# Kernel tuning notes

Measured on AMD Instinct MI355X. Metric: run time of the kernel, lower is better.

## Reference

```python
import jax, jax.numpy as jnp
import numpy as np
from jax import lax

# Static problem configuration (SAModule(ratio=0.25, r=0.2, MLP([35,64,64,128])))
B, N, C_IN = 8, 4096, 32
RATIO, R, K = 0.25, 0.2, 64   # K == max_num_neighbors
M = int(N * RATIO)            # centroids per cloud after FPS
NEG = -1e10


def setup_inputs() -> dict:
    key = jax.random.key(0)
    ks = jax.random.split(key, 6)
    x = jax.random.normal(ks[0], (B * N, C_IN), jnp.float32)
    pos = jax.random.uniform(ks[1], (B * N, 3), jnp.float32)  # unit cube -> r=0.2 balls are non-trivial
    batch = jnp.repeat(jnp.arange(B, dtype=jnp.int32), N)
    def lin(k, fan_in, fan_out):
        return jax.random.normal(k, (fan_in, fan_out), jnp.float32) * (1.0 / np.sqrt(fan_in))
    W1 = lin(ks[2], C_IN + 3, 64); b1 = jnp.zeros((64,), jnp.float32)
    W2 = lin(ks[3], 64, 64);       b2 = jnp.zeros((64,), jnp.float32)
    W3 = lin(ks[4], 64, 128);      b3 = jnp.zeros((128,), jnp.float32)
    return {"x": x, "pos": pos, "batch": batch,
            "W1": W1, "b1": b1, "W2": W2, "b2": b2, "W3": W3, "b3": b3}


def _fps_one(p):
    """Farthest-point sampling on one cloud p:[N,3] -> idx:[M] (deterministic start at 0)."""
    def body(carry, _):
        dmin, last = carry
        d = jnp.sum((p - p[last]) ** 2, axis=-1)         # [N] sq-dist to last picked point
        dmin = jnp.minimum(dmin, d)
        nxt = jnp.argmax(dmin).astype(jnp.int32)
        return (dmin, nxt), nxt
    init = (jnp.full((N,), 1e10, jnp.float32), jnp.int32(0))
    _, rest = lax.scan(body, init, None, length=M - 1)
    return jnp.concatenate([jnp.zeros((1,), jnp.int32), rest])


def _sa_one(p, xb, ib, W1, b1, W2, b2, W3, b3):
    """Radius ball-query + PointNetConv (gather -> MLP -> masked scatter-max) on one cloud."""
    ctr = p[ib]                                              # [M,3] sampled centroids
    d2 = jnp.sum((ctr[:, None, :] - p[None, :, :]) ** 2, -1)  # [M,N]
    negd, nbr = lax.top_k(-d2, K)                            # K nearest per centroid
    valid = (-negd) <= R * R                                 # inside-ball mask [M,K]
    xj = xb[nbr]                                             # [M,K,C_IN] gathered features
    rel = p[nbr] - ctr[:, None, :]                           # [M,K,3] relative positions
    h = jnp.concatenate([xj, rel], axis=-1)                  # message input [x_j, pos_j - pos_i]
    h = jax.nn.relu(h @ W1 + b1)
    h = jax.nn.relu(h @ W2 + b2)
    h = h @ W3 + b3                                          # plain last layer (PyG MLP plain_last)
    h = jnp.where(valid[..., None], h, NEG)
    return jnp.max(h, axis=1)                                # max aggregation -> [M,128]


def reference(x, pos, batch, W1, b1, W2, b2, W3, b3):
    pos3 = pos.reshape(B, N, 3)
    x3 = x.reshape(B, N, C_IN)
    idx = jax.vmap(_fps_one)(pos3)                           # [B,M]
    conv = lambda p, xb, ib: _sa_one(p, xb, ib, W1, b1, W2, b2, W3, b3)
    x_out = jax.vmap(conv)(pos3, x3, idx)                    # [B,M,128]
    pos_out = jnp.take_along_axis(pos3, idx[..., None], axis=1)  # [B,M,3]
    batch_out = jnp.repeat(jnp.arange(B, dtype=batch.dtype), M)
    return x_out.reshape(B * M, -1), pos_out.reshape(B * M, 3), batch_out
```

## Files before the change

kernel.cpp:

```cpp
#include <hip/hip_runtime.h>
#include <hip/hip_bf16.h>

#define BB 8
#define NN 4096
#define CIN 32
#define MM 1024
#define KNB 64
#define CAND 1024
#define ROWS 72
#define GRID 256
#define NWORK (GRID - 8)

typedef __attribute__((ext_vector_type(8))) short  short8;
typedef __attribute__((ext_vector_type(4))) float  f32x4;
typedef __attribute__((ext_vector_type(2))) float  f32x2;

__device__ __forceinline__ float sq3(float dx, float dy, float dz) {
    return __fadd_rn(__fadd_rn(__fmul_rn(dx, dx), __fmul_rn(dy, dy)), __fmul_rn(dz, dz));
}

__device__ __forceinline__ unsigned short f2bf(float v) {
    union { __hip_bfloat16 b; unsigned short u; } cv;
    cv.b = __float2bfloat16(v);
    return cv.u;
}
__device__ __forceinline__ float bf2f(unsigned short u) {
    union { unsigned short u; __hip_bfloat16 b; } cv;
    cv.u = u;
    return __bfloat162float(cv.b);
}

static __device__ __forceinline__ f32x4 mfma16(short8 a, short8 b, f32x4 c) {
    return __builtin_amdgcn_mfma_f32_16x16x32_bf16(a, b, c, 0, 0, 0);
}

template<int CTRL>
__device__ __forceinline__ unsigned long long dpp_maxkey(unsigned long long k) {
    unsigned int lo = (unsigned int)k;
    unsigned int hi = (unsigned int)(k >> 32);
    unsigned int nlo = (unsigned int)__builtin_amdgcn_update_dpp((int)lo, (int)lo, CTRL, 0xF, 0xF, false);
    unsigned int nhi = (unsigned int)__builtin_amdgcn_update_dpp((int)hi, (int)hi, CTRL, 0xF, 0xF, false);
    unsigned long long nk = ((unsigned long long)nhi << 32) | (unsigned long long)nlo;
    return nk > k ? nk : k;
}

__global__ __launch_bounds__(256) void prep_kernel(
    const float* __restrict__ W1, const float* __restrict__ W2,
    const float* __restrict__ W3, unsigned short* __restrict__ wf)
{
    int gid = blockIdx.x * 256 + threadIdx.x;
    const float* W; int K, Ncol, base, slot;
    if (gid < 1024)      { W = W1; K = 35; Ncol = 64;  base = 0;     slot = gid; }
    else if (gid < 2048) { W = W2; K = 64; Ncol = 64;  base = 8192;  slot = gid - 1024; }
    else                 { W = W3; K = 64; Ncol = 128; base = 16384; slot = gid - 2048; }
    int lane = slot & 63, h = (slot >> 6) & 1, kstep = (slot >> 7) & 1, tile = slot >> 8;
    int col = tile * 16 + (lane & 15), quad = lane >> 4;
#pragma unroll
    for (int j = 0; j < 8; ++j) {
        int k = kstep * 32 + quad * 8 + j;
        float wv = (k < K) ? W[k * Ncol + col] : 0.0f;
        unsigned short hi = f2bf(wv);
        unsigned short v = h ? f2bf(wv - bf2f(hi)) : hi;
        wf[base + slot * 8 + j] = v;
    }
}

struct SaShared {
    unsigned short HA[2 * 64 * ROWS];
    unsigned long long candk[CAND];
    int   cnt;
    int   ok;
    int   sel[KNB];
    float red[4][128];
};

__device__ __forceinline__ void sa_process(
    SaShared& sh, const float* __restrict__ x, const float* __restrict__ P,
    const unsigned short* __restrict__ wf,
    const float* __restrict__ b1, const float* __restrict__ b2,
    const float* __restrict__ b3, float* __restrict__ out, int bm, int b, int ci)
{
    const int t    = threadIdx.x;
    const int w    = t >> 6;
    const int lane = t & 63;
    const float R2 = (float)(0.2 * 0.2);

    if (t == 0) sh.cnt = 0;
    __syncthreads();

    const float cx = P[3 * ci], cy = P[3 * ci + 1], cz = P[3 * ci + 2];

    for (int i = t; i < NN; i += 256) {
        float dx = P[3 * i] - cx, dy = P[3 * i + 1] - cy, dz = P[3 * i + 2] - cz;
        float d2 = sq3(dx, dy, dz);
        bool hit = d2 <= R2;
        unsigned long long mk = __ballot(hit);
        if (mk) {
            int leader = __ffsll((unsigned long long)mk) - 1;
            int base = 0;
            if (lane == leader) base = atomicAdd(&sh.cnt, __popcll(mk));
            base = __shfl(base, leader);
            if (hit) {
                int p = base + __popcll(mk & ((1ull << lane) - 1));
                if (p < CAND)
                    sh.candk[p] = ((unsigned long long)__float_as_uint(d2) << 32)
                                | (unsigned int)i;
            }
        }
    }
    __syncthreads();
    const int n = min(sh.cnt, CAND);
    const int V = min(n, KNB);

    for (int i = t; i < n; i += 256) {
        unsigned long long ki = sh.candk[i];
        int rank = 0;
        for (int j = 0; j < n; ++j)
            rank += (sh.candk[j] < ki) ? 1 : 0;
        if (rank < KNB) sh.sel[rank] = (int)(ki & 0xffffffffu);
    }
    __syncthreads();

    {
        const int row = 16 * w + (lane & 15);
        const int prt = lane >> 4;
        short8 z = {};
        *(short8*)(sh.HA + row * ROWS + 32 + prt * 8) = z;
        *(short8*)(sh.HA + 64 * ROWS + row * ROWS + 32 + prt * 8) = z;
        if (row < V) {
            int g = b * NN + sh.sel[row];
            const float4* xr = (const float4*)(x + (size_t)g * CIN + prt * 8);
            float4 v0 = xr[0], v1 = xr[1];
            float vv[8] = {v0.x, v0.y, v0.z, v0.w, v1.x, v1.y, v1.z, v1.w};
            short8 hv, lv;
#pragma unroll
            for (int j = 0; j < 8; ++j) {
                unsigned short h = f2bf(vv[j]);
                hv[j] = (short)h;
                lv[j] = (short)f2bf(vv[j] - bf2f(h));
            }
            *(short8*)(sh.HA + row * ROWS + prt * 8) = hv;
            *(short8*)(sh.HA + 64 * ROWS + row * ROWS + prt * 8) = lv;
            if (prt == 0) {
                int g2 = sh.sel[row];
#pragma unroll
                for (int c = 0; c < 3; ++c) {
                    float cc = (c == 0) ? cx : (c == 1) ? cy : cz;
                    float rv = P[3 * g2 + c] - cc;
                    unsigned short h = f2bf(rv);
                    sh.HA[row * ROWS + 32 + c] = h;
                    sh.HA[64 * ROWS + row * ROWS + 32 + c] = f2bf(rv - bf2f(h));
                }
            }
        }
    }

    const int m16  = lane & 15;
    const int quad = lane >> 4;
    const int arow = 16 * w + m16;
    const short8* wf8 = (const short8*)wf;

    {
        short8 aH[2], aL[2];
        aH[0] = *(const short8*)(sh.HA + arow * ROWS + quad * 8);
        aH[1] = *(const short8*)(sh.HA + arow * ROWS + 32 + quad * 8);
        aL[0] = *(const short8*)(sh.HA + 64 * ROWS + arow * ROWS + quad * 8);
        aL[1] = *(const short8*)(sh.HA + 64 * ROWS + arow * ROWS + 32 + quad * 8);
#pragma unroll
        for (int tile = 0; tile < 4; ++tile) {
            f32x4 acc = {};
#pragma unroll
            for (int ks = 0; ks < 2; ++ks) {
                short8 bH = wf8[((tile * 2 + ks) * 2 + 0) * 64 + lane];
                short8 bL = wf8[((tile * 2 + ks) * 2 + 1) * 64 + lane];
                acc = mfma16(aH[ks], bH, acc);
                acc = mfma16(aH[ks], bL, acc);
                acc = mfma16(aL[ks], bH, acc);
            }
            int col = tile * 16 + m16;
            float bb = b1[col];
#pragma unroll
            for (int i = 0; i < 4; ++i) {
                int grow = 16 * w + quad * 4 + i;
                float v = fmaxf(acc[i] + bb, 0.0f);
                unsigned short h = f2bf(v);
                sh.HA[grow * ROWS + col] = h;
                sh.HA[64 * ROWS + grow * ROWS + col] = f2bf(v - bf2f(h));
            }
        }
    }

    {
        short8 aH[2], aL[2];
        aH[0] = *(const short8*)(sh.HA + arow * ROWS + quad * 8);
        aH[1] = *(const short8*)(sh.HA + arow * ROWS + 32 + quad * 8);
        aL[0] = *(const short8*)(sh.HA + 64 * ROWS + arow * ROWS + quad * 8);
        aL[1] = *(const short8*)(sh.HA + 64 * ROWS + arow * ROWS + 32 + quad * 8);
#pragma unroll
        for (int tile = 0; tile < 4; ++tile) {
            f32x4 acc = {};
#pragma unroll
            for (int ks = 0; ks < 2; ++ks) {
                short8 bH = wf8[1024 + ((tile * 2 + ks) * 2 + 0) * 64 + lane];
                short8 bL = wf8[1024 + ((tile * 2 + ks) * 2 + 1) * 64 + lane];
                acc = mfma16(aH[ks], bH, acc);
                acc = mfma16(aH[ks], bL, acc);
                acc = mfma16(aL[ks], bH, acc);
            }
            int col = tile * 16 + m16;
            float bb = b2[col];
#pragma unroll
            for (int i = 0; i < 4; ++i) {
                int grow = 16 * w + quad * 4 + i;
                float v = fmaxf(acc[i] + bb, 0.0f);
                unsigned short h = f2bf(v);
                sh.HA[grow * ROWS + col] = h;
                sh.HA[64 * ROWS + grow * ROWS + col] = f2bf(v - bf2f(h));
            }
        }
    }

    {
        short8 aH[2], aL[2];
        aH[0] = *(const short8*)(sh.HA + arow * ROWS + quad * 8);
        aH[1] = *(const short8*)(sh.HA + arow * ROWS + 32 + quad * 8);
        aL[0] = *(const short8*)(sh.HA + 64 * ROWS + arow * ROWS + quad * 8);
        aL[1] = *(const short8*)(sh.HA + 64 * ROWS + arow * ROWS + 32 + quad * 8);
#pragma unroll
        for (int tile = 0; tile < 8; ++tile) {
            f32x4 acc = {};
#pragma unroll
            for (int ks = 0; ks < 2; ++ks) {
                short8 bH = wf8[2048 + ((tile * 2 + ks) * 2 + 0) * 64 + lane];
                short8 bL = wf8[2048 + ((tile * 2 + ks) * 2 + 1) * 64 + lane];
                acc = mfma16(aH[ks], bH, acc);
                acc = mfma16(aH[ks], bL, acc);
                acc = mfma16(aL[ks], bH, acc);
            }
            float mv = -1e10f;
#pragma unroll
            for (int i = 0; i < 4; ++i) {
                int grow = 16 * w + quad * 4 + i;
                float v = (grow < V) ? acc[i] : -1e10f;
                mv = fmaxf(mv, v);
            }
            mv = fmaxf(mv, __shfl_xor(mv, 16));
            mv = fmaxf(mv, __shfl_xor(mv, 32));
            if (lane < 16) sh.red[w][tile * 16 + lane] = mv;
        }
    }
    __syncthreads();

    if (t < 128) {
        float v = fmaxf(fmaxf(sh.red[0][t], sh.red[1][t]),
                        fmaxf(sh.red[2][t], sh.red[3][t]));
        out[(size_t)bm * 128 + t] = v + b3[t];
    }
}

union SharedMem {
    struct {
        float4 plds4[NN];
        int    chosen[MM];
        __align__(16) unsigned long long part[2][4];
    } fps;
    SaShared sa;
    char occupancy_pad[86016];
};

__global__ __launch_bounds__(256, 1) void fused_kernel(
    const float* __restrict__ x, const float* __restrict__ pos,
    int* __restrict__ idx_ws, unsigned int* __restrict__ ready,
    int* __restrict__ done, const unsigned short* __restrict__ wf,
    const float* __restrict__ b1, const float* __restrict__ b2,
    const float* __restrict__ b3, float* __restrict__ out)
{
    __shared__ SharedMem sh;
    const int t = threadIdx.x;

    if (blockIdx.x < BB) {
        __builtin_amdgcn_s_setprio(3);
        const int b = blockIdx.x;
        const float* P = pos + (size_t)b * NN * 3;
        for (int i = t; i < NN; i += 256) {
            float4 v;
            v.x = P[3 * i]; v.y = P[3 * i + 1]; v.z = P[3 * i + 2]; v.w = 0.0f;
            sh.fps.plds4[i] = v;
        }
        if (t == 0) {
            sh.fps.chosen[0] = 0;
            __hip_atomic_store(&idx_ws[b * MM], 0, __ATOMIC_RELAXED,
                               __HIP_MEMORY_SCOPE_AGENT);
        }
        __syncthreads();

        f32x2 pxv[8], pyv[8], pzv[8], dminv[8];
#pragma unroll
        for (int s = 0; s < 8; ++s) {
            float4 a = sh.fps.plds4[t + 512 * s];
            float4 c = sh.fps.plds4[t + 512 * s + 256];
            pxv[s] = (f32x2){a.x, c.x};
            pyv[s] = (f32x2){a.y, c.y};
            pzv[s] = (f32x2){a.z, c.z};
            dminv[s] = (f32x2){1e10f, 1e10f};
        }

        int win = 0;
        for (int it = 1; it < MM; ++it) {
            float4 wc = sh.fps.plds4[win];
            const f32x2 lxv = (f32x2){wc.x, wc.x};
            const f32x2 lyv = (f32x2){wc.y, wc.y};
            const f32x2 lzv = (f32x2){wc.z, wc.z};
            float bv = -1.0f;
            int   bi = 0;
#pragma unroll
            for (int s = 0; s < 8; ++s) {
                f32x2 d;
                {
#pragma clang fp contract(off)
                    f32x2 dx = pxv[s] - lxv;
                    f32x2 dy = pyv[s] - lyv;
                    f32x2 dz = pzv[s] - lzv;
                    d = dx * dx + dy * dy + dz * dz;
                }
                float m0 = fminf(dminv[s].x, d.x);
                float m1 = fminf(dminv[s].y, d.y);
                dminv[s].x = m0;
                dminv[s].y = m1;
                if (m0 > bv) { bv = m0; bi = t + 512 * s; }
                if (m1 > bv) { bv = m1; bi = t + 512 * s + 256; }
            }
            unsigned long long k =
                ((unsigned long long)__float_as_uint(bv) << 32) | (unsigned int)(~bi);
            k = dpp_maxkey<0x111>(k);
            k = dpp_maxkey<0x112>(k);
            k = dpp_maxkey<0x114>(k);
            k = dpp_maxkey<0x118>(k);
            k = dpp_maxkey<0x142>(k);
            k = dpp_maxkey<0x143>(k);
            if ((t & 63) == 63) sh.fps.part[it & 1][t >> 6] = k;
            __syncthreads();
            const ulonglong2* pp = (const ulonglong2*)&sh.fps.part[it & 1][0];
            ulonglong2 p01 = pp[0], p23 = pp[1];
            unsigned long long ka = p01.x > p01.y ? p01.x : p01.y;
            unsigned long long kb = p23.x > p23.y ? p23.x : p23.y;
            unsigned long long km = ka > kb ? ka : kb;
            win = (int)(~(unsigned int)km);
            if (t == 0) {
                sh.fps.chosen[it] = win;
                __hip_atomic_store(&idx_ws[b * MM + it], win, __ATOMIC_RELAXED,
                                   __HIP_MEMORY_SCOPE_AGENT);
                if ((it & 31) == 31)
                    __hip_atomic_store(&ready[b], (unsigned int)(it + 1),
                                       __ATOMIC_RELEASE, __HIP_MEMORY_SCOPE_AGENT);
            }
        }
        __syncthreads();

        for (int m = t; m < MM; m += 256) {
            int mi = sh.fps.chosen[m];
            const int PO = BB * MM * 128;
            const int BO = PO + BB * MM * 3;
            int row = b * MM + m;
            float4 c = sh.fps.plds4[mi];
            out[PO + 3 * row + 0] = c.x;
            out[PO + 3 * row + 1] = c.y;
            out[PO + 3 * row + 2] = c.z;
            out[BO + row] = (float)b;
        }
        return;
    }

    int budget = 8000;
    for (int item = (int)blockIdx.x - BB; item < BB * MM; item += NWORK) {
        const int m  = item >> 3;
        const int b  = item & 7;
        const int bm = b * MM + m;
        const float* P = pos + (size_t)b * NN * 3;

        if (t == 0) {
            const unsigned int need = (unsigned int)(m + 1);
            while (budget > 0 &&
                   __hip_atomic_load(&ready[b], __ATOMIC_ACQUIRE,
                                     __HIP_MEMORY_SCOPE_AGENT) < need) {
                __builtin_amdgcn_s_sleep(10);
                --budget;
            }
            sh.sa.ok = (__hip_atomic_load(&ready[b], __ATOMIC_ACQUIRE,
                                          __HIP_MEMORY_SCOPE_AGENT) >= need) ? 1 : 0;
        }
        __syncthreads();
        const int myok = sh.sa.ok;
        __syncthreads();
        if (!myok) continue;

        const int ci = __hip_atomic_load(&idx_ws[bm], __ATOMIC_RELAXED,
                                         __HIP_MEMORY_SCOPE_AGENT) & (NN - 1);
        sa_process(sh.sa, x, P, wf, b1, b2, b3, out, bm, b, ci);
        if (t == 0)
            __hip_atomic_store(&done[bm], 1, __ATOMIC_RELAXED,
                               __HIP_MEMORY_SCOPE_AGENT);
    }
}

__global__ __launch_bounds__(256, 4) void sweep_kernel(
    const float* __restrict__ x, const float* __restrict__ pos,
    const int* __restrict__ idx_ws, const int* __restrict__ done,
    const unsigned short* __restrict__ wf,
    const float* __restrict__ b1, const float* __restrict__ b2,
    const float* __restrict__ b3, float* __restrict__ out)
{
    __shared__ SaShared sh;
    const int bm = blockIdx.x;
    if (done[bm]) return;
    const int b = bm >> 10;
    const float* P = pos + (size_t)b * NN * 3;
    const int ci = idx_ws[bm] & (NN - 1);
    sa_process(sh, x, P, wf, b1, b2, b3, out, bm, b, ci);
}

extern "C" void kernel_launch(void* const* d_in, const int* in_sizes, int n_in,
                              void* d_out, int out_size, void* d_ws, size_t ws_size,
                              hipStream_t stream) {
    const float* x   = (const float*)d_in[0];
    const float* pos = (const float*)d_in[1];
    const float* W1 = (const float*)d_in[3];
    const float* b1 = (const float*)d_in[4];
    const float* W2 = (const float*)d_in[5];
    const float* b2 = (const float*)d_in[6];
    const float* W3 = (const float*)d_in[7];
    const float* b3 = (const float*)d_in[8];
    float* out    = (float*)d_out;
    int*   idx_ws = (int*)d_ws;
    unsigned short* wf = (unsigned short*)((char*)d_ws + 32768);
    unsigned int* ready = (unsigned int*)((char*)d_ws + 98304);
    int* done = (int*)((char*)d_ws + 98368);

    hipMemsetAsync((char*)d_ws + 98304, 0, 131136 - 98304, stream);
    hipLaunchKernelGGL(prep_kernel, dim3(16), dim3(256), 0, stream, W1, W2, W3, wf);
    hipLaunchKernelGGL(fused_kernel, dim3(GRID), dim3(256), 0, stream,
                       x, pos, idx_ws, ready, done, wf, b1, b2, b3, out);
    hipLaunchKernelGGL(sweep_kernel, dim3(BB * MM), dim3(256), 0, stream,
                       x, pos, idx_ws, done, wf, b1, b2, b3, out);
}
```

Before: 712.0 us.

## Fold weight prep into fused kernel, pack FPS math in asm, batch sweep blocks

The separate weight-prep kernel launch is removed. Block BB of the fused kernel now builds the bf16 split weights and publishes them through a release flag, and every worker block spins on that flag before starting. The FPS distance loop uses explicit v_pk_add/v_pk_mul inline asm with negated centroid coordinates, which keeps unfused arithmetic while forcing packed instructions. The sweep kernel launches 512 blocks that each loop over 16 items, down from one block per item, which cuts launch and early-exit block overhead. In exchange, one worker block is delayed by the weight prep and all worker blocks gain a spin-wait.

```diff
diff --git a/kernel.cpp b/kernel.cpp
--- a/kernel.cpp
+++ b/kernel.cpp
@@ -19,6 +19,13 @@
     return __fadd_rn(__fadd_rn(__fmul_rn(dx, dx), __fmul_rn(dy, dy)), __fmul_rn(dz, dz));
 }
 
+__device__ __forceinline__ f32x2 pk_add(f32x2 a, f32x2 b) {
+    f32x2 d; asm("v_pk_add_f32 %0, %1, %2" : "=v"(d) : "v"(a), "v"(b)); return d;
+}
+__device__ __forceinline__ f32x2 pk_mul(f32x2 a, f32x2 b) {
+    f32x2 d; asm("v_pk_mul_f32 %0, %1, %2" : "=v"(d) : "v"(a), "v"(b)); return d;
+}
+
 __device__ __forceinline__ unsigned short f2bf(float v) {
     union { __hip_bfloat16 b; unsigned short u; } cv;
     cv.b = __float2bfloat16(v);
@@ -42,27 +49,6 @@
     unsigned int nhi = (unsigned int)__builtin_amdgcn_update_dpp((int)hi, (int)hi, CTRL, 0xF, 0xF, false);
     unsigned long long nk = ((unsigned long long)nhi << 32) | (unsigned long long)nlo;
     return nk > k ? nk : k;
-}
-
-__global__ __launch_bounds__(256) void prep_kernel(
-    const float* __restrict__ W1, const float* __restrict__ W2,
-    const float* __restrict__ W3, unsigned short* __restrict__ wf)
-{
-    int gid = blockIdx.x * 256 + threadIdx.x;
-    const float* W; int K, Ncol, base, slot;
-    if (gid < 1024)      { W = W1; K = 35; Ncol = 64;  base = 0;     slot = gid; }
-    else if (gid < 2048) { W = W2; K = 64; Ncol = 64;  base = 8192;  slot = gid - 1024; }
-    else                 { W = W3; K = 64; Ncol = 128; base = 16384; slot = gid - 2048; }
-    int lane = slot & 63, h = (slot >> 6) & 1, kstep = (slot >> 7) & 1, tile = slot >> 8;
-    int col = tile * 16 + (lane & 15), quad = lane >> 4;
-#pragma unroll
-    for (int j = 0; j < 8; ++j) {
-        int k = kstep * 32 + quad * 8 + j;
-        float wv = (k < K) ? W[k * Ncol + col] : 0.0f;
-        unsigned short hi = f2bf(wv);
-        unsigned short v = h ? f2bf(wv - bf2f(hi)) : hi;
-        wf[base + slot * 8 + j] = v;
-    }
 }
 
 struct SaShared {
@@ -271,7 +257,9 @@
 __global__ __launch_bounds__(256, 1) void fused_kernel(
     const float* __restrict__ x, const float* __restrict__ pos,
     int* __restrict__ idx_ws, unsigned int* __restrict__ ready,
-    int* __restrict__ done, const unsigned short* __restrict__ wf,
+    unsigned int* __restrict__ wfflag, int* __restrict__ done,
+    const float* __restrict__ W1, const float* __restrict__ W2,
+    const float* __restrict__ W3, unsigned short* __restrict__ wf,
     const float* __restrict__ b1, const float* __restrict__ b2,
     const float* __restrict__ b3, float* __restrict__ out)
 {
@@ -308,21 +296,18 @@
         int win = 0;
         for (int it = 1; it < MM; ++it) {
             float4 wc = sh.fps.plds4[win];
-            const f32x2 lxv = (f32x2){wc.x, wc.x};
-            const f32x2 lyv = (f32x2){wc.y, wc.y};
-            const f32x2 lzv = (f32x2){wc.z, wc.z};
+            const f32x2 lxn = (f32x2){-wc.x, -wc.x};
+            const f32x2 lyn = (f32x2){-wc.y, -wc.y};
+            const f32x2 lzn = (f32x2){-wc.z, -wc.z};
             float bv = -1.0f;
             int   bi = 0;
 #pragma unroll
             for (int s = 0; s < 8; ++s) {
-                f32x2 d;
-                {
-#pragma clang fp contract(off)
-                    f32x2 dx = pxv[s] - lxv;
-                    f32x2 dy = pyv[s] - lyv;
-                    f32x2 dz = pzv[s] - lzv;
-                    d = dx * dx + dy * dy + dz * dz;
-                }
+                f32x2 dx = pk_add(pxv[s], lxn);
+                f32x2 dy = pk_add(pyv[s], lyn);
+                f32x2 dz = pk_add(pzv[s], lzn);
+                f32x2 d  = pk_add(pk_add(pk_mul(dx, dx), pk_mul(dy, dy)),
+                                  pk_mul(dz, dz));
                 float m0 = fminf(dminv[s].x, d.x);
                 float m1 = fminf(dminv[s].y, d.y);
                 dminv[s].x = m0;
@@ -371,6 +356,35 @@
         return;
     }
 
+    if (blockIdx.x == BB) {
+        for (int gid = t; gid < 4096; gid += 256) {
+            const float* W; int K, Ncol, base, slot;
+            if (gid < 1024)      { W = W1; K = 35; Ncol = 64;  base = 0;     slot = gid; }
+            else if (gid < 2048) { W = W2; K = 64; Ncol = 64;  base = 8192;  slot = gid - 1024; }
+            else                 { W = W3; K = 64; Ncol = 128; base = 16384; slot = gid - 2048; }
+            int lane2 = slot & 63, h2 = (slot >> 6) & 1, kstep = (slot >> 7) & 1, tile = slot >> 8;
+            int col = tile * 16 + (lane2 & 15), quad2 = lane2 >> 4;
+#pragma unroll
+            for (int j = 0; j < 8; ++j) {
+                int k = kstep * 32 + quad2 * 8 + j;
+                float wv = (k < K) ? W[k * Ncol + col] : 0.0f;
+                unsigned short hi = f2bf(wv);
+                unsigned short v = h2 ? f2bf(wv - bf2f(hi)) : hi;
+                wf[base + slot * 8 + j] = v;
+            }
+        }
+        __syncthreads();
+        if (t == 0)
+            __hip_atomic_store(wfflag, 1u, __ATOMIC_RELEASE,
+                               __HIP_MEMORY_SCOPE_AGENT);
+    }
+    if (t == 0) {
+        while (__hip_atomic_load(wfflag, __ATOMIC_ACQUIRE,
+                                 __HIP_MEMORY_SCOPE_AGENT) == 0)
+            __builtin_amdgcn_s_sleep(2);
+    }
+    __syncthreads();
+
     int budget = 8000;
     for (int item = (int)blockIdx.x - BB; item < BB * MM; item += NWORK) {
         const int m  = item >> 3;
@@ -411,12 +425,15 @@
     const float* __restrict__ b3, float* __restrict__ out)
 {
     __shared__ SaShared sh;
-    const int bm = blockIdx.x;
-    if (done[bm]) return;
-    const int b = bm >> 10;
-    const float* P = pos + (size_t)b * NN * 3;
-    const int ci = idx_ws[bm] & (NN - 1);
-    sa_process(sh, x, P, wf, b1, b2, b3, out, bm, b, ci);
+    for (int j = 0; j < 16; ++j) {
+        __syncthreads();
+        const int bm = blockIdx.x * 16 + j;
+        if (done[bm]) continue;
+        const int b = bm >> 10;
+        const float* P = pos + (size_t)b * NN * 3;
+        const int ci = idx_ws[bm] & (NN - 1);
+        sa_process(sh, x, P, wf, b1, b2, b3, out, bm, b, ci);
+    }
 }
 
 extern "C" void kernel_launch(void* const* d_in, const int* in_sizes, int n_in,
@@ -434,12 +451,13 @@
     int*   idx_ws = (int*)d_ws;
     unsigned short* wf = (unsigned short*)((char*)d_ws + 32768);
     unsigned int* ready = (unsigned int*)((char*)d_ws + 98304);
+    unsigned int* wfflag = (unsigned int*)((char*)d_ws + 98336);
     int* done = (int*)((char*)d_ws + 98368);
 
     hipMemsetAsync((char*)d_ws + 98304, 0, 131136 - 98304, stream);
-    hipLaunchKernelGGL(prep_kernel, dim3(16), dim3(256), 0, stream, W1, W2, W3, wf);
     hipLaunchKernelGGL(fused_kernel, dim3(GRID), dim3(256), 0, stream,
-                       x, pos, idx_ws, ready, done, wf, b1, b2, b3, out);
-    hipLaunchKernelGGL(sweep_kernel, dim3(BB * MM), dim3(256), 0, stream,
+                       x, pos, idx_ws, ready, wfflag, done,
+                       W1, W2, W3, wf, b1, b2, b3, out);
+    hipLaunchKernelGGL(sweep_kernel, dim3(512), dim3(256), 0, stream,
                        x, pos, idx_ws, done, wf, b1, b2, b3, out);
 }
```

After: 846.3 us. 18.9% more time.
